# Kernel tuning notes

Measured on AMD Instinct MI355X. Metric: run time of the kernel, lower is better.

Reference implementation:

```python
import jax, jax.numpy as jnp
import numpy as np

N = 100_000          # nodes
E = 3_200_000        # edges (avg degree 32)
DIMS = [6, 20, 15, 10, 5, 2]


def setup_inputs() -> dict:
    key = jax.random.key(0)
    ks = jax.random.split(key, 3 + 2 * 5)
    inp = {
        "x": jax.random.normal(ks[0], (N, DIMS[0]), jnp.float32),
        "edge_index": jax.random.randint(ks[1], (2, E), 0, N, jnp.int32),
        "edge_weight": jax.random.uniform(ks[2], (E,), jnp.float32),
    }
    for i in range(5):
        din, dout = DIMS[i], DIMS[i + 1]
        s = 1.0 / np.sqrt(din)
        inp[f"w_rel{i}"] = jax.random.normal(ks[3 + 2 * i], (din, dout), jnp.float32) * s
        inp[f"b_rel{i}"] = jnp.zeros((dout,), jnp.float32)
        inp[f"w_root{i}"] = jax.random.normal(ks[4 + 2 * i], (din, dout), jnp.float32) * s
    return inp


def _graph_conv(x, src, dst, w, W_rel, b_rel, W_root):
    # PyG GraphConv: lin_rel(scatter_add(w_e * x_src)) + lin_root(x)
    msg = x[src] * w[:, None]                                  # [E, din]
    agg = jax.ops.segment_sum(msg, dst, num_segments=N)        # [N, din]
    return agg @ W_rel + b_rel + x @ W_root                    # [N, dout]


def reference(x, edge_index, edge_weight,
              w_rel0, b_rel0, w_root0,
              w_rel1, b_rel1, w_root1,
              w_rel2, b_rel2, w_root2,
              w_rel3, b_rel3, w_root3,
              w_rel4, b_rel4, w_root4):
    src, dst = edge_index[0], edge_index[1]
    layers = [
        (w_rel0, b_rel0, w_root0),
        (w_rel1, b_rel1, w_root1),
        (w_rel2, b_rel2, w_root2),
        (w_rel3, b_rel3, w_root3),
        (w_rel4, b_rel4, w_root4),
    ]
    for W_rel, b_rel, W_root in layers:
        x = jax.nn.relu(_graph_conv(x, src, dst, edge_weight, W_rel, b_rel, W_root))
    return jax.nn.softmax(x, axis=1)
```

## Files before the change

### kernel.cpp

```cpp
#include <hip/hip_runtime.h>
#include <hip/hip_fp16.h>
#include <stdint.h>

#define N_NODES 100000
#define N_EDGES 3200000
#define BN      64
#define NB      1563
#define NCH_H   1024
#define CH_H    (N_EDGES / NCH_H)
#define CPL     (NCH_H / 64)
#define PAD_PER 98
#define NCH_S   256
#define CH_S    (N_EDGES / NCH_S)
#define BS1     1024
#define S1_IT   ((CH_S + BS1 - 1) / BS1)
#define S2_CAP  2560
#define BLOCK   256
#define W_SCALE 32767.0f
#define W_INV   (1.0f / 32767.0f)

__global__ void hist_kernel(const int* __restrict__ dst, int* __restrict__ hist_g,
                            const float* __restrict__ x, __half* __restrict__ xpad) {
    __shared__ int h[NB];
    for (int b = threadIdx.x; b < NB; b += BLOCK) h[b] = 0;
    {
        int i = blockIdx.x * PAD_PER + threadIdx.x;
        if (threadIdx.x < PAD_PER && i < N_NODES) {
            const float* xr = x + (size_t)i * 6;
            __half2 hh[4];
            hh[0] = __halves2half2(__float2half(xr[0]), __float2half(xr[1]));
            hh[1] = __halves2half2(__float2half(xr[2]), __float2half(xr[3]));
            hh[2] = __halves2half2(__float2half(xr[4]), __float2half(xr[5]));
            hh[3] = __halves2half2(__float2half(0.f),   __float2half(0.f));
            *(uint4*)(xpad + (size_t)i * 8) = *(uint4*)hh;
        }
    }
    __syncthreads();
    const int c  = blockIdx.x;
    const int k0 = c * CH_H;
    for (int k = threadIdx.x; k < CH_H; k += BLOCK)
        atomicAdd(&h[dst[k0 + k] >> 6], 1);
    __syncthreads();
    for (int b = threadIdx.x; b < NB; b += BLOCK)
        hist_g[c * NB + b] = h[b];
}

__global__ void chunkscan_kernel(const int* __restrict__ hist_g,
                                 int* __restrict__ off_g, int* __restrict__ tot) {
    int w    = (blockIdx.x * blockDim.x + threadIdx.x) >> 6;
    int lane = threadIdx.x & 63;
    if (w >= NB) return;
    int v[CPL];
    int ls = 0;
    const int cbase = lane * CPL;
    #pragma unroll
    for (int i = 0; i < CPL; ++i) { v[i] = hist_g[(cbase + i) * NB + w]; ls += v[i]; }
    int run = ls;
    #pragma unroll
    for (int d = 1; d < 64; d <<= 1) {
        int u = __shfl_up(run, d);
        if (lane >= d) run += u;
    }
    int acc = run - ls;
    #pragma unroll
    for (int i = 0; i < CPL; ++i) { off_g[(cbase + i) * NB + w] = acc; acc += v[i]; }
    if (lane == 63) tot[w] = acc;
}

#define SCAN_T   1024
#define SCAN_PER 2
__global__ void scan_kernel(const int* __restrict__ cnt, int* __restrict__ bstart) {
    __shared__ int part[SCAN_T];
    int t = threadIdx.x;
    int local[SCAN_PER];
    int s = 0;
    #pragma unroll
    for (int i = 0; i < SCAN_PER; ++i) {
        int idx = t * SCAN_PER + i;
        int v = (idx < NB) ? cnt[idx] : 0;
        local[i] = s;
        s += v;
    }
    part[t] = s;
    __syncthreads();
    for (int off = 1; off < SCAN_T; off <<= 1) {
        int v = (t >= off) ? part[t - off] : 0;
        __syncthreads();
        part[t] += v;
        __syncthreads();
    }
    int excl = part[t] - s;
    #pragma unroll
    for (int i = 0; i < SCAN_PER; ++i) {
        int idx = t * SCAN_PER + i;
        if (idx < NB) bstart[idx] = excl + local[i];
    }
}

__global__ void __launch_bounds__(BS1)
scatter1_kernel(const int* __restrict__ src, const int* __restrict__ dst,
                const float* __restrict__ w,
                const int* __restrict__ bstart, const int* __restrict__ off_g,
                uint2* __restrict__ rec1) {
    __shared__ uint32_t stage[CH_S];
    __shared__ int h[NB];
    __shared__ int delta[NB];
    __shared__ int wtot[BS1 / 64];

    const int c  = blockIdx.x;
    const int k0 = c * CH_S;
    const int t  = threadIdx.x;

    for (int b = t; b < NB; b += BS1) h[b] = 0;
    __syncthreads();
    int dstv[S1_IT];
    int nit = 0;
    for (int k = t; k < CH_S; k += BS1, ++nit) {
        int d = dst[k0 + k];
        dstv[nit] = d;
        atomicAdd(&h[d >> 6], 1);
    }
    __syncthreads();

    {
        const int base = t * 2;
        int v[2], ls = 0;
        #pragma unroll
        for (int i = 0; i < 2; ++i) {
            int idx = base + i;
            v[i] = (idx < NB) ? h[idx] : 0;
            ls += v[i];
        }
        int lane = t & 63, wv = t >> 6;
        int run = ls;
        #pragma unroll
        for (int d = 1; d < 64; d <<= 1) {
            int u = __shfl_up(run, d);
            if (lane >= d) run += u;
        }
        if (lane == 63) wtot[wv] = run;
        __syncthreads();
        int wexcl = 0;
        for (int i = 0; i < wv; ++i) wexcl += wtot[i];
        int excl = wexcl + run - ls;
        #pragma unroll
        for (int i = 0; i < 2; ++i) {
            int idx = base + i;
            if (idx < NB) {
                int gb = bstart[idx] + off_g[(size_t)(4 * c) * NB + idx];
                h[idx]     = excl;
                delta[idx] = gb - excl;
                excl += v[i];
            }
        }
    }
    __syncthreads();

    nit = 0;
    for (int k = t; k < CH_S; k += BS1, ++nit) {
        int d = dstv[nit];
        int b = d >> 6;
        int pos = atomicAdd(&h[b], 1);
        stage[pos] = (uint32_t)k | ((uint32_t)(d & 63) << 14) | ((uint32_t)b << 20);
    }
    __syncthreads();

    for (int i = t; i < CH_S; i += 4 * BS1) {
        uint32_t sv[4];
        #pragma unroll
        for (int u = 0; u < 4; ++u) {
            int ii = i + u * BS1;
            sv[u] = (ii < CH_S) ? stage[ii] : 0u;
        }
        uint32_t ssrc[4], sw[4];
        #pragma unroll
        for (int u = 0; u < 4; ++u) {
            int e = k0 + (int)(sv[u] & 0x3FFF);
            ssrc[u] = (uint32_t)src[e];
            sw[u]   = __float_as_uint(w[e]);
        }
        #pragma unroll
        for (int u = 0; u < 4; ++u) {
            int ii = i + u * BS1;
            if (ii < CH_S) {
                uint2 r;
                r.x = ssrc[u] | (((sv[u] >> 14) & 0x3F) << 17);
                r.y = sw[u];
                rec1[delta[sv[u] >> 20] + ii] = r;
            }
        }
    }
}

__global__ void scatter2_kernel(const uint2* __restrict__ rec1,
                                const int* __restrict__ bstart, const int* __restrict__ tot,
                                uint32_t* __restrict__ rec2,
                                int* __restrict__ row_start, int* __restrict__ cnt) {
    __shared__ int h[BN];
    __shared__ int cur[BN];
    __shared__ uint32_t stage[S2_CAP];
    const int b  = blockIdx.x;
    const int s0 = bstart[b];
    const int n  = tot[b];
    if (threadIdx.x < BN) h[threadIdx.x] = 0;
    __syncthreads();
    for (int k = threadIdx.x; k < n; k += BLOCK)
        atomicAdd(&h[rec1[s0 + k].x >> 17], 1);
    __syncthreads();
    if (threadIdx.x < BN) {
        int v = h[threadIdx.x];
        int run = v;
        #pragma unroll
        for (int d = 1; d < 64; d <<= 1) {
            int u = __shfl_up(run, d);
            if (threadIdx.x >= d) run += u;
        }
        int excl = run - v;
        cur[threadIdx.x] = excl;
        int node = b * BN + threadIdx.x;
        if (node < N_NODES) { row_start[node] = s0 + excl; cnt[node] = v; }
    }
    __syncthreads();
    for (int k = threadIdx.x; k < n; k += BLOCK) {
        uint2 r = rec1[s0 + k];
        int dl = (int)(r.x >> 17);
        float wv = __uint_as_float(r.y);
        uint32_t w15 = (uint32_t)__float2uint_rn(wv * W_SCALE);
        uint32_t r2 = (r.x & 0x1FFFF) | (w15 << 17);
        int pos = atomicAdd(&cur[dl], 1);
        if (pos < S2_CAP) stage[pos] = r2;
        else              rec2[s0 + pos] = r2;
    }
    __syncthreads();
    for (int i = threadIdx.x; i < n && i < S2_CAP; i += BLOCK)
        rec2[s0 + i] = stage[i];
}

__global__ void layer0_kernel(const __half* __restrict__ xpad,
                              const uint32_t* __restrict__ rec,
                              const int* __restrict__ row_start, const int* __restrict__ cnt,
                              const float* __restrict__ wrel0, const float* __restrict__ brel0,
                              const float* __restrict__ wroot0,
                              const float* __restrict__ wrel1, const float* __restrict__ brel1,
                              const float* __restrict__ wroot1,
                              __half* __restrict__ pn, float* __restrict__ oinitn) {
    __shared__ float s_wrel0[6 * 20], s_wroot0[6 * 20], s_b0[20];
    __shared__ float s_wrel1[20 * 15], s_wroot1[20 * 15], s_b1[15];
    for (int t = threadIdx.x; t < 120; t += BLOCK) {
        s_wrel0[t]  = wrel0[t];
        s_wroot0[t] = wroot0[t];
    }
    for (int t = threadIdx.x; t < 300; t += BLOCK) {
        s_wrel1[t]  = wrel1[t];
        s_wroot1[t] = wroot1[t];
    }
    if (threadIdx.x < 20) s_b0[threadIdx.x] = brel0[threadIdx.x];
    if (threadIdx.x < 15) s_b1[threadIdx.x] = brel1[threadIdx.x];
    __syncthreads();

    int t = blockIdx.x * blockDim.x + threadIdx.x;
    int node = t >> 3;
    int q    = t & 7;

    float agg[6] = {0.f, 0.f, 0.f, 0.f, 0.f, 0.f};
    const int s = row_start[node];
    const int e = s + cnt[node];
    for (int k = s + q; k < e; k += 32) {
        uint32_t rv[4];
        float    wv[4];
        #pragma unroll
        for (int u = 0; u < 4; ++u) {
            int kk = k + 8 * u;
            int kc = kk < e ? kk : (e - 1);
            rv[u] = rec[kc];
            wv[u] = kk < e ? (float)(rv[u] >> 17) * W_INV : 0.f;
        }
        uint4 raw[4];
        #pragma unroll
        for (int u = 0; u < 4; ++u)
            raw[u] = *(const uint4*)(xpad + (size_t)(rv[u] & 0x1FFFF) * 8);
        #pragma unroll
        for (int u = 0; u < 4; ++u) {
            const __half2* h = (const __half2*)&raw[u];
            float w = wv[u];
            agg[0] += w * __low2float(h[0]);  agg[1] += w * __high2float(h[0]);
            agg[2] += w * __low2float(h[1]);  agg[3] += w * __high2float(h[1]);
            agg[4] += w * __low2float(h[2]);  agg[5] += w * __high2float(h[2]);
        }
    }
    #pragma unroll
    for (int i = 0; i < 6; ++i) {
        agg[i] += __shfl_xor(agg[i], 1);
        agg[i] += __shfl_xor(agg[i], 2);
        agg[i] += __shfl_xor(agg[i], 4);
    }
    uint4 raws = *(const uint4*)(xpad + (size_t)node * 8);
    const __half2* hs = (const __half2*)&raws;
    float xv[6] = { __low2float(hs[0]), __high2float(hs[0]),
                    __low2float(hs[1]), __high2float(hs[1]),
                    __low2float(hs[2]), __high2float(hs[2]) };
    float ov[20];
    #pragma unroll
    for (int j = 0; j < 20; ++j) {
        float o = s_b0[j];
        #pragma unroll
        for (int i = 0; i < 6; ++i)
            o += agg[i] * s_wrel0[i * 20 + j] + xv[i] * s_wroot0[i * 20 + j];
        ov[j] = fmaxf(o, 0.f);
    }
    {
        float pk[2] = {0.f, 0.f};
        #pragma unroll
        for (int kk = 0; kk < 2; ++kk) {
            int k = 2 * q + kk;
            if (k < 15) {
                float sacc = 0.f;
                #pragma unroll
                for (int j = 0; j < 20; ++j) sacc += ov[j] * s_wrel1[j * 15 + k];
                pk[kk] = sacc;
            }
        }
        ((__half2*)(pn + (size_t)node * 16))[q] =
            __halves2half2(__float2half(pk[0]), __float2half(pk[1]));
    }
    #pragma unroll
    for (int kk = 0; kk < 2; ++kk) {
        int k = q + kk * 8;
        if (k < 15) {
            float sacc = s_b1[k];
            #pragma unroll
            for (int j = 0; j < 20; ++j) sacc += ov[j] * s_wroot1[j * 15 + k];
            oinitn[(size_t)node * 15 + k] = sacc;
        }
    }
}

template<int DOUT, int SPH, int NDOUT, int NSPH, bool LAST>
__global__ void gather_kernel(const __half* __restrict__ p, const float* __restrict__ oinit,
                              const uint32_t* __restrict__ rec,
                              const int* __restrict__ row_start, const int* __restrict__ cnt,
                              const float* __restrict__ wrel_n, const float* __restrict__ brel_n,
                              const float* __restrict__ wroot_n,
                              __half* __restrict__ pn, float* __restrict__ oinitn,
                              float* __restrict__ out) {
    __shared__ float s_wrel[LAST ? 1 : DOUT * NDOUT];
    __shared__ float s_wroot[LAST ? 1 : DOUT * NDOUT];
    __shared__ float s_b[LAST ? 1 : (NDOUT > 0 ? NDOUT : 1)];
    if constexpr (!LAST) {
        for (int t = threadIdx.x; t < DOUT * NDOUT; t += BLOCK) {
            s_wrel[t]  = wrel_n[t];
            s_wroot[t] = wroot_n[t];
        }
        if (threadIdx.x < NDOUT) s_b[threadIdx.x] = brel_n[threadIdx.x];
        __syncthreads();
    }

    int t = blockIdx.x * blockDim.x + threadIdx.x;
    int node = t >> 3;
    int q    = t & 7;

    float af[SPH];
    #pragma unroll
    for (int i = 0; i < SPH; ++i) af[i] = 0.f;

    const int s = row_start[node];
    const int e = s + cnt[node];
    constexpr int NR = (SPH >= 8) ? SPH / 8 : 1;
    for (int k = s + q; k < e; k += 32) {
        uint32_t rv[4];
        float    wv[4];
        #pragma unroll
        for (int u = 0; u < 4; ++u) {
            int kk = k + 8 * u;
            int kc = kk < e ? kk : (e - 1);
            rv[u] = rec[kc];
            wv[u] = kk < e ? (float)(rv[u] >> 17) * W_INV : 0.f;
        }
        if constexpr (SPH >= 8) {
            uint4 raw[4 * NR];
            #pragma unroll
            for (int u = 0; u < 4; ++u) {
                const uint4* ps = (const uint4*)(p + (size_t)(rv[u] & 0x1FFFF) * SPH);
                #pragma unroll
                for (int v = 0; v < NR; ++v) raw[u * NR + v] = ps[v];
            }
            #pragma unroll
            for (int u = 0; u < 4; ++u) {
                float w = wv[u];
                #pragma unroll
                for (int v = 0; v < NR; ++v) {
                    const __half2* h = (const __half2*)&raw[u * NR + v];
                    #pragma unroll
                    for (int jj = 0; jj < 4; ++jj) {
                        af[v * 8 + 2 * jj]     += w * __low2float(h[jj]);
                        af[v * 8 + 2 * jj + 1] += w * __high2float(h[jj]);
                    }
                }
            }
        } else {
            uint32_t raw[4];
            #pragma unroll
            for (int u = 0; u < 4; ++u)
                raw[u] = *(const uint32_t*)(p + (size_t)(rv[u] & 0x1FFFF) * SPH);
            #pragma unroll
            for (int u = 0; u < 4; ++u) {
                __half2 h = *(const __half2*)&raw[u];
                af[0] += wv[u] * __low2float(h);
                af[1] += wv[u] * __high2float(h);
            }
        }
    }
    #pragma unroll
    for (int i = 0; i < SPH; ++i) {
        af[i] += __shfl_xor(af[i], 1);
        af[i] += __shfl_xor(af[i], 2);
        af[i] += __shfl_xor(af[i], 4);
    }

    if constexpr (LAST) {
        if (q == 0) {
            float o0 = af[0] + oinit[(size_t)node * 2 + 0];
            float o1 = af[1] + oinit[(size_t)node * 2 + 1];
            float m = fmaxf(o0, o1);
            float e0 = __expf(o0 - m), e1 = __expf(o1 - m);
            float inv = 1.f / (e0 + e1);
            out[(size_t)node * 2 + 0] = e0 * inv;
            out[(size_t)node * 2 + 1] = e1 * inv;
        }
    } else {
        float ov[DOUT];
        #pragma unroll
        for (int j = 0; j < DOUT; ++j)
            ov[j] = fmaxf(af[j] + oinit[(size_t)node * DOUT + j], 0.f);

        if (q < NSPH / 2) {
            float pk[2] = {0.f, 0.f};
            #pragma unroll
            for (int kk = 0; kk < 2; ++kk) {
                int k = 2 * q + kk;
                if (k < NDOUT) {
                    float sacc = 0.f;
                    #pragma unroll
                    for (int j = 0; j < DOUT; ++j) sacc += ov[j] * s_wrel[j * NDOUT + k];
                    pk[kk] = sacc;
                }
            }
            ((__half2*)(pn + (size_t)node * NSPH))[q] =
                __halves2half2(__float2half(pk[0]), __float2half(pk[1]));
        }
        #pragma unroll
        for (int kk = 0; kk < 2; ++kk) {
            int k = q + kk * 8;
            if (k < NDOUT) {
                float sacc = s_b[k];
                #pragma unroll
                for (int j = 0; j < DOUT; ++j) sacc += ov[j] * s_wroot[j * NDOUT + k];
                oinitn[(size_t)node * NDOUT + k] = sacc;
            }
        }
    }
}


extern "C" void kernel_launch(void* const* d_in, const int* in_sizes, int n_in,
                              void* d_out, int out_size, void* d_ws, size_t ws_size,
                              hipStream_t stream) {
    const float* x  = (const float*)d_in[0];
    const int*   ei = (const int*)d_in[1];
    const float* ew = (const float*)d_in[2];
    const float* wrel[5]  = { (const float*)d_in[3], (const float*)d_in[6],
                              (const float*)d_in[9], (const float*)d_in[12],
                              (const float*)d_in[15] };
    const float* brel[5]  = { (const float*)d_in[4], (const float*)d_in[7],
                              (const float*)d_in[10], (const float*)d_in[13],
                              (const float*)d_in[16] };
    const float* wroot[5] = { (const float*)d_in[5], (const float*)d_in[8],
                              (const float*)d_in[11], (const float*)d_in[14],
                              (const float*)d_in[17] };

    char* ws = (char*)d_ws;
    size_t off = 0;
    auto alloc = [&](size_t bytes) -> void* {
        void* ptr = ws + off;
        off += (bytes + 255) & ~(size_t)255;
        return ptr;
    };
    char*     regionA   = (char*)alloc((size_t)N_EDGES * 8);
    uint2*    rec1      = (uint2*)regionA;
    __half*   pA        = (__half*)regionA;
    __half*   pB        = (__half*)(regionA + (size_t)4  * 1024 * 1024);
    float*    oA        = (float*)(regionA + (size_t)8  * 1024 * 1024);
    float*    oB        = (float*)(regionA + (size_t)16 * 1024 * 1024);
    uint32_t* rec2      = (uint32_t*)alloc((size_t)N_EDGES * 4);
    __half*   xpad      = (__half*)alloc((size_t)N_NODES * 8 * 2);
    int*      hist_g    = (int*)alloc((size_t)NCH_H * NB * 4);
    int*      off_g     = (int*)alloc((size_t)NCH_H * NB * 4);
    int*      tot       = (int*)alloc((size_t)NB * 4);
    int*      bstart    = (int*)alloc((size_t)NB * 4);
    int*      row_start = (int*)alloc((size_t)N_NODES * 4);
    int*      cntb      = (int*)alloc((size_t)N_NODES * 4);

    const int* srcv = ei;
    const int* dstv = ei + N_EDGES;

    const int gN8 = (8 * N_NODES + BLOCK - 1) / BLOCK;

    hist_kernel     <<<NCH_H, BLOCK, 0, stream>>>(dstv, hist_g, x, xpad);
    chunkscan_kernel<<<(NB + 3) / 4, BLOCK, 0, stream>>>(hist_g, off_g, tot);
    scan_kernel     <<<1, SCAN_T, 0, stream>>>(tot, bstart);
    scatter1_kernel <<<NCH_S, BS1, 0, stream>>>(srcv, dstv, ew, bstart, off_g, rec1);
    scatter2_kernel <<<NB, BLOCK, 0, stream>>>(rec1, bstart, tot, rec2, row_start, cntb);

    layer0_kernel<<<gN8, BLOCK, 0, stream>>>(xpad, rec2, row_start, cntb,
                                             wrel[0], brel[0], wroot[0],
                                             wrel[1], brel[1], wroot[1], pA, oA);
    gather_kernel<15, 16, 10, 16, false><<<gN8, BLOCK, 0, stream>>>(
        pA, oA, rec2, row_start, cntb, wrel[2], brel[2], wroot[2], pB, oB, nullptr);
    gather_kernel<10, 16, 5, 8, false><<<gN8, BLOCK, 0, stream>>>(
        pB, oB, rec2, row_start, cntb, wrel[3], brel[3], wroot[3], pA, oA, nullptr);
    gather_kernel<5, 8, 2, 2, false><<<gN8, BLOCK, 0, stream>>>(
        pA, oA, rec2, row_start, cntb, wrel[4], brel[4], wroot[4], pB, oB, nullptr);
    gather_kernel<2, 2, 0, 0, true><<<gN8, BLOCK, 0, stream>>>(
        pB, oB, rec2, row_start, cntb, nullptr, nullptr, nullptr,
        nullptr, nullptr, (float*)d_out);
}
```

Measured before the change: 320.7 us.

## Fuse second scatter pass with layer-0 gather using shared-memory edge records

Merges scatter2 and layer0 into one kernel so each block, after bucketing its 64 destination nodes' edges into shared memory, immediately aggregates layer 0 from the staged records instead of re-reading rec2 from global memory. Work mapping changes from 8 threads per node to 4 threads per node, with each thread covering more output slots. The workspace no longer aliases rec1 with the p/o buffers, since rec1 and the layer outputs are now live at the same time. This removes one launch and a global re-read of the edge list, but halves per-node parallelism in the layer-0 gather and adds shared-memory pressure.

```diff
diff --git a/kernel.cpp b/kernel.cpp
--- a/kernel.cpp
+++ b/kernel.cpp
@@ -192,21 +192,46 @@
     }
 }
 
-__global__ void scatter2_kernel(const uint2* __restrict__ rec1,
-                                const int* __restrict__ bstart, const int* __restrict__ tot,
-                                uint32_t* __restrict__ rec2,
-                                int* __restrict__ row_start, int* __restrict__ cnt) {
+__global__ void scatter2_layer0_kernel(
+        const uint2* __restrict__ rec1,
+        const int* __restrict__ bstart, const int* __restrict__ tot,
+        uint32_t* __restrict__ rec2,
+        int* __restrict__ row_start, int* __restrict__ cnt,
+        const __half* __restrict__ xpad,
+        const float* __restrict__ wrel0, const float* __restrict__ brel0,
+        const float* __restrict__ wroot0,
+        const float* __restrict__ wrel1, const float* __restrict__ brel1,
+        const float* __restrict__ wroot1,
+        __half* __restrict__ pn, float* __restrict__ oinitn) {
     __shared__ int h[BN];
     __shared__ int cur[BN];
-    __shared__ uint32_t stage[S2_CAP];
+    __shared__ int seg[BN];
+    __shared__ int segc[BN];
+    __shared__ uint32_t sout[S2_CAP];
+    __shared__ float s_wrel0[6 * 20], s_wroot0[6 * 20], s_b0[20];
+    __shared__ float s_wrel1[20 * 15], s_wroot1[20 * 15], s_b1[15];
+
     const int b  = blockIdx.x;
     const int s0 = bstart[b];
     const int n  = tot[b];
+
+    for (int t = threadIdx.x; t < 120; t += BLOCK) {
+        s_wrel0[t]  = wrel0[t];
+        s_wroot0[t] = wroot0[t];
+    }
+    for (int t = threadIdx.x; t < 300; t += BLOCK) {
+        s_wrel1[t]  = wrel1[t];
+        s_wroot1[t] = wroot1[t];
+    }
+    if (threadIdx.x < 20) s_b0[threadIdx.x] = brel0[threadIdx.x];
+    if (threadIdx.x < 15) s_b1[threadIdx.x] = brel1[threadIdx.x];
     if (threadIdx.x < BN) h[threadIdx.x] = 0;
     __syncthreads();
+
     for (int k = threadIdx.x; k < n; k += BLOCK)
         atomicAdd(&h[rec1[s0 + k].x >> 17], 1);
     __syncthreads();
+
     if (threadIdx.x < BN) {
         int v = h[threadIdx.x];
         int run = v;
@@ -216,11 +241,14 @@
             if (threadIdx.x >= d) run += u;
         }
         int excl = run - v;
-        cur[threadIdx.x] = excl;
+        seg[threadIdx.x]  = excl;
+        segc[threadIdx.x] = v;
+        cur[threadIdx.x]  = excl;
         int node = b * BN + threadIdx.x;
         if (node < N_NODES) { row_start[node] = s0 + excl; cnt[node] = v; }
     }
     __syncthreads();
+
     for (int k = threadIdx.x; k < n; k += BLOCK) {
         uint2 r = rec1[s0 + k];
         int dl = (int)(r.x >> 17);
@@ -228,52 +256,30 @@
         uint32_t w15 = (uint32_t)__float2uint_rn(wv * W_SCALE);
         uint32_t r2 = (r.x & 0x1FFFF) | (w15 << 17);
         int pos = atomicAdd(&cur[dl], 1);
-        if (pos < S2_CAP) stage[pos] = r2;
+        if (pos < S2_CAP) sout[pos] = r2;
         else              rec2[s0 + pos] = r2;
     }
     __syncthreads();
+
     for (int i = threadIdx.x; i < n && i < S2_CAP; i += BLOCK)
-        rec2[s0 + i] = stage[i];
-}
-
-__global__ void layer0_kernel(const __half* __restrict__ xpad,
-                              const uint32_t* __restrict__ rec,
-                              const int* __restrict__ row_start, const int* __restrict__ cnt,
-                              const float* __restrict__ wrel0, const float* __restrict__ brel0,
-                              const float* __restrict__ wroot0,
-                              const float* __restrict__ wrel1, const float* __restrict__ brel1,
-                              const float* __restrict__ wroot1,
-                              __half* __restrict__ pn, float* __restrict__ oinitn) {
-    __shared__ float s_wrel0[6 * 20], s_wroot0[6 * 20], s_b0[20];
-    __shared__ float s_wrel1[20 * 15], s_wroot1[20 * 15], s_b1[15];
-    for (int t = threadIdx.x; t < 120; t += BLOCK) {
-        s_wrel0[t]  = wrel0[t];
-        s_wroot0[t] = wroot0[t];
-    }
-    for (int t = threadIdx.x; t < 300; t += BLOCK) {
-        s_wrel1[t]  = wrel1[t];
-        s_wroot1[t] = wroot1[t];
-    }
-    if (threadIdx.x < 20) s_b0[threadIdx.x] = brel0[threadIdx.x];
-    if (threadIdx.x < 15) s_b1[threadIdx.x] = brel1[threadIdx.x];
-    __syncthreads();
-
-    int t = blockIdx.x * blockDim.x + threadIdx.x;
-    int node = t >> 3;
-    int q    = t & 7;
+        rec2[s0 + i] = sout[i];
+
+    const int ln = threadIdx.x >> 2;
+    const int q  = threadIdx.x & 3;
+    const int node = b * BN + ln;
 
     float agg[6] = {0.f, 0.f, 0.f, 0.f, 0.f, 0.f};
-    const int s = row_start[node];
-    const int e = s + cnt[node];
-    for (int k = s + q; k < e; k += 32) {
+    const int ss = seg[ln];
+    const int ee = ss + segc[ln];
+    for (int k = ss + q; k < ee; k += 16) {
         uint32_t rv[4];
         float    wv[4];
         #pragma unroll
         for (int u = 0; u < 4; ++u) {
-            int kk = k + 8 * u;
-            int kc = kk < e ? kk : (e - 1);
-            rv[u] = rec[kc];
-            wv[u] = kk < e ? (float)(rv[u] >> 17) * W_INV : 0.f;
+            int kk = k + 4 * u;
+            int kc = kk < ee ? kk : (ee - 1);
+            rv[u] = (kc < S2_CAP) ? sout[kc] : rec2[s0 + kc];
+            wv[u] = kk < ee ? (float)(rv[u] >> 17) * W_INV : 0.f;
         }
         uint4 raw[4];
         #pragma unroll
@@ -281,19 +287,20 @@
             raw[u] = *(const uint4*)(xpad + (size_t)(rv[u] & 0x1FFFF) * 8);
         #pragma unroll
         for (int u = 0; u < 4; ++u) {
-            const __half2* h = (const __half2*)&raw[u];
+            const __half2* hh = (const __half2*)&raw[u];
             float w = wv[u];
-            agg[0] += w * __low2float(h[0]);  agg[1] += w * __high2float(h[0]);
-            agg[2] += w * __low2float(h[1]);  agg[3] += w * __high2float(h[1]);
-            agg[4] += w * __low2float(h[2]);  agg[5] += w * __high2float(h[2]);
+            agg[0] += w * __low2float(hh[0]);  agg[1] += w * __high2float(hh[0]);
+            agg[2] += w * __low2float(hh[1]);  agg[3] += w * __high2float(hh[1]);
+            agg[4] += w * __low2float(hh[2]);  agg[5] += w * __high2float(hh[2]);
         }
     }
     #pragma unroll
     for (int i = 0; i < 6; ++i) {
         agg[i] += __shfl_xor(agg[i], 1);
         agg[i] += __shfl_xor(agg[i], 2);
-        agg[i] += __shfl_xor(agg[i], 4);
-    }
+    }
+    if (node >= N_NODES) return;
+
     uint4 raws = *(const uint4*)(xpad + (size_t)node * 8);
     const __half2* hs = (const __half2*)&raws;
     float xv[6] = { __low2float(hs[0]), __high2float(hs[0]),
@@ -308,11 +315,13 @@
             o += agg[i] * s_wrel0[i * 20 + j] + xv[i] * s_wroot0[i * 20 + j];
         ov[j] = fmaxf(o, 0.f);
     }
-    {
+    #pragma unroll
+    for (int sl = 0; sl < 2; ++sl) {
+        int slot = q + sl * 4;
         float pk[2] = {0.f, 0.f};
         #pragma unroll
         for (int kk = 0; kk < 2; ++kk) {
-            int k = 2 * q + kk;
+            int k = 2 * slot + kk;
             if (k < 15) {
                 float sacc = 0.f;
                 #pragma unroll
@@ -320,12 +329,12 @@
                 pk[kk] = sacc;
             }
         }
-        ((__half2*)(pn + (size_t)node * 16))[q] =
+        ((__half2*)(pn + (size_t)node * 16))[slot] =
             __halves2half2(__float2half(pk[0]), __float2half(pk[1]));
     }
     #pragma unroll
-    for (int kk = 0; kk < 2; ++kk) {
-        int k = q + kk * 8;
+    for (int kk = 0; kk < 4; ++kk) {
+        int k = q + kk * 4;
         if (k < 15) {
             float sacc = s_b1[k];
             #pragma unroll
@@ -485,13 +494,12 @@
         off += (bytes + 255) & ~(size_t)255;
         return ptr;
     };
-    char*     regionA   = (char*)alloc((size_t)N_EDGES * 8);
-    uint2*    rec1      = (uint2*)regionA;
-    __half*   pA        = (__half*)regionA;
-    __half*   pB        = (__half*)(regionA + (size_t)4  * 1024 * 1024);
-    float*    oA        = (float*)(regionA + (size_t)8  * 1024 * 1024);
-    float*    oB        = (float*)(regionA + (size_t)16 * 1024 * 1024);
+    uint2*    rec1      = (uint2*)alloc((size_t)N_EDGES * 8);
     uint32_t* rec2      = (uint32_t*)alloc((size_t)N_EDGES * 4);
+    __half*   pA        = (__half*)alloc((size_t)N_NODES * 16 * 2);
+    __half*   pB        = (__half*)alloc((size_t)N_NODES * 16 * 2);
+    float*    oA        = (float*)alloc((size_t)N_NODES * 15 * 4);
+    float*    oB        = (float*)alloc((size_t)N_NODES * 15 * 4);
     __half*   xpad      = (__half*)alloc((size_t)N_NODES * 8 * 2);
     int*      hist_g    = (int*)alloc((size_t)NCH_H * NB * 4);
     int*      off_g     = (int*)alloc((size_t)NCH_H * NB * 4);
@@ -509,11 +517,11 @@
     chunkscan_kernel<<<(NB + 3) / 4, BLOCK, 0, stream>>>(hist_g, off_g, tot);
     scan_kernel     <<<1, SCAN_T, 0, stream>>>(tot, bstart);
     scatter1_kernel <<<NCH_S, BS1, 0, stream>>>(srcv, dstv, ew, bstart, off_g, rec1);
-    scatter2_kernel <<<NB, BLOCK, 0, stream>>>(rec1, bstart, tot, rec2, row_start, cntb);
-
-    layer0_kernel<<<gN8, BLOCK, 0, stream>>>(xpad, rec2, row_start, cntb,
-                                             wrel[0], brel[0], wroot[0],
-                                             wrel[1], brel[1], wroot[1], pA, oA);
+
+    scatter2_layer0_kernel<<<NB, BLOCK, 0, stream>>>(
+        rec1, bstart, tot, rec2, row_start, cntb, xpad,
+        wrel[0], brel[0], wroot[0], wrel[1], brel[1], wroot[1], pA, oA);
+
     gather_kernel<15, 16, 10, 16, false><<<gN8, BLOCK, 0, stream>>>(
         pA, oA, rec2, row_start, cntb, wrel[2], brel[2], wroot[2], pB, oB, nullptr);
     gather_kernel<10, 16, 5, 8, false><<<gN8, BLOCK, 0, stream>>>(
```

Result: no change. 323.9 us (+1.0%).

## Sort nodes by in-degree so gather warps process balanced work

Applied to the files above, without the earlier changes.

Builds a degree histogram in scatter2, scans it in descending degree order, and places nodes into a permutation grouped by degree. All gather kernels then map each group of 8 threads to perm[node] instead of the node index, so waves hold nodes with similar edge counts and lose less time to divergence on loop trip counts. This adds three small kernels, a memset, and an extra indirection. It also scatters accesses to row_start, cnt, oinit and the outputs, since neighbouring threads now handle unrelated node ids.

```diff
diff --git a/kernel.cpp b/kernel.cpp
--- a/kernel.cpp
+++ b/kernel.cpp
@@ -16,6 +16,7 @@
 #define S1_IT   ((CH_S + BS1 - 1) / BS1)
 #define S2_CAP  2560
 #define BLOCK   256
+#define DEGB    128
 #define W_SCALE 32767.0f
 #define W_INV   (1.0f / 32767.0f)
 
@@ -195,7 +196,8 @@
 __global__ void scatter2_kernel(const uint2* __restrict__ rec1,
                                 const int* __restrict__ bstart, const int* __restrict__ tot,
                                 uint32_t* __restrict__ rec2,
-                                int* __restrict__ row_start, int* __restrict__ cnt) {
+                                int* __restrict__ row_start, int* __restrict__ cnt,
+                                int* __restrict__ degh) {
     __shared__ int h[BN];
     __shared__ int cur[BN];
     __shared__ uint32_t stage[S2_CAP];
@@ -218,7 +220,12 @@
         int excl = run - v;
         cur[threadIdx.x] = excl;
         int node = b * BN + threadIdx.x;
-        if (node < N_NODES) { row_start[node] = s0 + excl; cnt[node] = v; }
+        if (node < N_NODES) {
+            row_start[node] = s0 + excl;
+            cnt[node] = v;
+            int bin = v < DEGB ? v : DEGB - 1;
+            atomicAdd(&degh[bin], 1);
+        }
     }
     __syncthreads();
     for (int k = threadIdx.x; k < n; k += BLOCK) {
@@ -236,9 +243,44 @@
         rec2[s0 + i] = stage[i];
 }
 
+__global__ void degscan_kernel(const int* __restrict__ degh, int* __restrict__ cursor) {
+    __shared__ int sh[DEGB];
+    int t = threadIdx.x;
+    if (t < DEGB) sh[t] = degh[t];
+    __syncthreads();
+    if (t < DEGB) {
+        int s = 0;
+        for (int d = t + 1; d < DEGB; ++d) s += sh[d];
+        cursor[t] = s;
+    }
+}
+
+__global__ void place_kernel(const int* __restrict__ cnt, int* __restrict__ cursor,
+                             int* __restrict__ perm) {
+    __shared__ int lh[DEGB];
+    __shared__ int bb[DEGB];
+    int t = threadIdx.x;
+    for (int i = t; i < DEGB; i += BLOCK) lh[i] = 0;
+    __syncthreads();
+    int node = blockIdx.x * BLOCK + t;
+    int deg = 0, lrank = 0;
+    bool valid = node < N_NODES;
+    if (valid) {
+        deg = cnt[node];
+        if (deg > DEGB - 1) deg = DEGB - 1;
+        lrank = atomicAdd(&lh[deg], 1);
+    }
+    __syncthreads();
+    for (int i = t; i < DEGB; i += BLOCK)
+        bb[i] = lh[i] ? atomicAdd(&cursor[i], lh[i]) : 0;
+    __syncthreads();
+    if (valid) perm[bb[deg] + lrank] = node;
+}
+
 __global__ void layer0_kernel(const __half* __restrict__ xpad,
                               const uint32_t* __restrict__ rec,
                               const int* __restrict__ row_start, const int* __restrict__ cnt,
+                              const int* __restrict__ perm,
                               const float* __restrict__ wrel0, const float* __restrict__ brel0,
                               const float* __restrict__ wroot0,
                               const float* __restrict__ wrel1, const float* __restrict__ brel1,
@@ -259,7 +301,7 @@
     __syncthreads();
 
     int t = blockIdx.x * blockDim.x + threadIdx.x;
-    int node = t >> 3;
+    int node = perm[t >> 3];
     int q    = t & 7;
 
     float agg[6] = {0.f, 0.f, 0.f, 0.f, 0.f, 0.f};
@@ -339,6 +381,7 @@
 __global__ void gather_kernel(const __half* __restrict__ p, const float* __restrict__ oinit,
                               const uint32_t* __restrict__ rec,
                               const int* __restrict__ row_start, const int* __restrict__ cnt,
+                              const int* __restrict__ perm,
                               const float* __restrict__ wrel_n, const float* __restrict__ brel_n,
                               const float* __restrict__ wroot_n,
                               __half* __restrict__ pn, float* __restrict__ oinitn,
@@ -356,7 +399,7 @@
     }
 
     int t = blockIdx.x * blockDim.x + threadIdx.x;
-    int node = t >> 3;
+    int node = perm[t >> 3];
     int q    = t & 7;
 
     float af[SPH];
@@ -499,28 +542,36 @@
     int*      bstart    = (int*)alloc((size_t)NB * 4);
     int*      row_start = (int*)alloc((size_t)N_NODES * 4);
     int*      cntb      = (int*)alloc((size_t)N_NODES * 4);
+    int*      degh      = (int*)alloc((size_t)DEGB * 4);
+    int*      dcursor   = (int*)alloc((size_t)DEGB * 4);
+    int*      perm      = (int*)alloc((size_t)N_NODES * 4);
 
     const int* srcv = ei;
     const int* dstv = ei + N_EDGES;
 
     const int gN8 = (8 * N_NODES + BLOCK - 1) / BLOCK;
+
+    hipMemsetAsync(degh, 0, DEGB * 4, stream);
 
     hist_kernel     <<<NCH_H, BLOCK, 0, stream>>>(dstv, hist_g, x, xpad);
     chunkscan_kernel<<<(NB + 3) / 4, BLOCK, 0, stream>>>(hist_g, off_g, tot);
     scan_kernel     <<<1, SCAN_T, 0, stream>>>(tot, bstart);
     scatter1_kernel <<<NCH_S, BS1, 0, stream>>>(srcv, dstv, ew, bstart, off_g, rec1);
-    scatter2_kernel <<<NB, BLOCK, 0, stream>>>(rec1, bstart, tot, rec2, row_start, cntb);
-
-    layer0_kernel<<<gN8, BLOCK, 0, stream>>>(xpad, rec2, row_start, cntb,
+    scatter2_kernel <<<NB, BLOCK, 0, stream>>>(rec1, bstart, tot, rec2,
+                                               row_start, cntb, degh);
+    degscan_kernel  <<<1, DEGB, 0, stream>>>(degh, dcursor);
+    place_kernel    <<<(N_NODES + BLOCK - 1) / BLOCK, BLOCK, 0, stream>>>(cntb, dcursor, perm);
+
+    layer0_kernel<<<gN8, BLOCK, 0, stream>>>(xpad, rec2, row_start, cntb, perm,
                                              wrel[0], brel[0], wroot[0],
                                              wrel[1], brel[1], wroot[1], pA, oA);
     gather_kernel<15, 16, 10, 16, false><<<gN8, BLOCK, 0, stream>>>(
-        pA, oA, rec2, row_start, cntb, wrel[2], brel[2], wroot[2], pB, oB, nullptr);
+        pA, oA, rec2, row_start, cntb, perm, wrel[2], brel[2], wroot[2], pB, oB, nullptr);
     gather_kernel<10, 16, 5, 8, false><<<gN8, BLOCK, 0, stream>>>(
-        pB, oB, rec2, row_start, cntb, wrel[3], brel[3], wroot[3], pA, oA, nullptr);
+        pB, oB, rec2, row_start, cntb, perm, wrel[3], brel[3], wroot[3], pA, oA, nullptr);
     gather_kernel<5, 8, 2, 2, false><<<gN8, BLOCK, 0, stream>>>(
-        pA, oA, rec2, row_start, cntb, wrel[4], brel[4], wroot[4], pB, oB, nullptr);
+        pA, oA, rec2, row_start, cntb, perm, wrel[4], brel[4], wroot[4], pB, oB, nullptr);
     gather_kernel<2, 2, 0, 0, true><<<gN8, BLOCK, 0, stream>>>(
-        pB, oB, rec2, row_start, cntb, nullptr, nullptr, nullptr,
+        pB, oB, rec2, row_start, cntb, perm, nullptr, nullptr, nullptr,
         nullptr, nullptr, (float*)d_out);
 }
```

Result: slower. 529.7 us (+65.2%).
